# Optimization experiments

Measured on AMD Instinct MI355X. Metric: run time of the kernel, lower is better.

Reference implementation:

```python
import jax, jax.numpy as jnp
import numpy as np

TOP_K = 2
SCALING = 16.0 / 8.0  # alpha / rank


def setup_inputs() -> dict:
    key = jax.random.key(0)
    ks = jax.random.split(key, 9)
    B, V, D, P = 32, 21, 512, 64
    IN, OUT, E, R, H = D * P, 96, 8, 8, 256
    return {
        "x": jax.random.normal(ks[0], (B, V, D, P), jnp.float32),
        "W_base": jax.random.normal(ks[1], (OUT, IN), jnp.float32) * (IN ** -0.5),
        "b_base": jax.random.normal(ks[2], (OUT,), jnp.float32) * 0.01,
        "W1": jax.random.normal(ks[3], (H, D), jnp.float32) * (D ** -0.5),
        "b1": jax.random.normal(ks[4], (H,), jnp.float32) * 0.01,
        "W2": jax.random.normal(ks[5], (E, H), jnp.float32) * (H ** -0.5),
        "b2": jax.random.normal(ks[6], (E,), jnp.float32) * 0.01,
        "lora_A": jax.random.normal(ks[7], (E, R, IN), jnp.float32) * (IN ** -0.5),
        "lora_B": jax.random.normal(ks[8], (E, OUT, R), jnp.float32) * (R ** -0.5),
    }


def reference(x, W_base, b_base, W1, b1, W2, b2, lora_A, lora_B):
    B, V, D, P = x.shape
    E = lora_A.shape[0]
    # FlattenHead: flatten last two dims, then linear (dropout is identity in eval)
    flat = x.reshape(B, V, D * P)                      # [B, V, IN]
    base_out = flat @ W_base.T + b_base                # [B, V, OUT]
    # Router: pool over n_vars then patch dim -> [B, D]
    pooled = x.mean(axis=1).mean(axis=-1)
    h = jax.nn.relu(pooled @ W1.T + b1)
    logits = h @ W2.T + b2                             # [B, E]
    probs = jax.nn.softmax(logits, axis=-1)
    topw, topi = jax.lax.top_k(probs, TOP_K)           # [B, K]
    topw = topw / jnp.clip(topw.sum(-1, keepdims=True), 1e-6)
    # All LoRA experts (matches original dense compute), then weighted combine
    temp = jnp.einsum("bvi,eri->ebvr", flat, lora_A)   # [E, B, V, R]
    delta = jnp.einsum("ebvr,eor->ebvo", temp, lora_B) * SCALING  # [E, B, V, OUT]
    # Scatter top-k weights into dense [B, E] then combine (top-k sparse combine)
    w_full = jnp.zeros((B, E), x.dtype).at[jnp.arange(B)[:, None], topi].add(topw)
    moe_delta = jnp.einsum("be,ebvo->bvo", w_full, delta)
    return base_out + moe_delta, probs
```

## Files before the change

### kernel.cpp

```cpp
#include <hip/hip_runtime.h>

#define B_DIM 32
#define V_DIM 21
#define D_DIM 512
#define P_DIM 64
#define M_TOTAL 672
#define K_TOTAL 32768
#define OUT_DIM 96
#define E_DIM 8
#define R_DIM 8
#define H_DIM 256
#define N_TOTAL 160
#define SCALING 2.0f
#define POOL_SCALE (1.0f / (V_DIM * (float)P_DIM))

#define BM 64
#define BK 128
#define KSPLIT 32
#define K_PER_BLOCK (K_TOTAL / KSPLIT)
#define CHUNKS (K_PER_BLOCK / BK)
#define LDS_K (BK + 8)

typedef __attribute__((ext_vector_type(4))) float floatx4;
typedef __attribute__((ext_vector_type(8))) short short8;

__device__ __forceinline__ unsigned short f2bf(float f) {
  union { float f; unsigned int u; } v; v.f = f;
  unsigned int u = v.u + (0x7FFFu + ((v.u >> 16) & 1u));
  return (unsigned short)(u >> 16);
}

__global__ __launch_bounds__(256, 2)
void gemm_kernel(const float* __restrict__ x, const float* __restrict__ W_base,
                 const float* __restrict__ lora_A, float* __restrict__ S,
                 float* __restrict__ pooled) {
  __shared__ short ldsA[BM * LDS_K];
  __shared__ short ldsW[N_TOTAL * LDS_K];
  __shared__ float lds_pool[5 * 16];
  const int tid = threadIdx.x;
  const int m0 = blockIdx.x * BM;
  const int kbase = blockIdx.y * K_PER_BLOCK;
  const int lane = tid & 63;
  const int wave = tid >> 6;
  const int quad = lane >> 4;
  const int l16 = lane & 15;
  const int b_first = m0 / V_DIM;
  const int d_first = kbase >> 6;

  if (tid < 80) lds_pool[tid] = 0.0f;

  floatx4 acc[10];
  #pragma unroll
  for (int i = 0; i < 10; ++i) acc[i] = (floatx4)(0.0f);

  for (int c = 0; c < CHUNKS; ++c) {
    const int kc = kbase + c * BK;
    __syncthreads();
    #pragma unroll
    for (int it = 0; it < 4; ++it) {
      int idx = it * 256 + tid;
      int row = idx >> 4;
      int g = idx & 15;
      int m = m0 + row;
      float vals[8];
      if (m < M_TOTAL) {
        const floatx4* s4 = (const floatx4*)(x + (size_t)m * K_TOTAL + kc + g * 8);
        floatx4 v0 = s4[0], v1 = s4[1];
        vals[0] = v0[0]; vals[1] = v0[1]; vals[2] = v0[2]; vals[3] = v0[3];
        vals[4] = v1[0]; vals[5] = v1[1]; vals[6] = v1[2]; vals[7] = v1[3];
        float sum8 = (vals[0] + vals[1]) + (vals[2] + vals[3]) +
                     ((vals[4] + vals[5]) + (vals[6] + vals[7]));
        int b_local = (m / V_DIM) - b_first;
        int d_local = ((kc + g * 8) >> 6) - d_first;
        atomicAdd(&lds_pool[b_local * 16 + d_local], sum8);
      } else {
        #pragma unroll
        for (int j = 0; j < 8; ++j) vals[j] = 0.0f;
      }
      short8 sv;
      #pragma unroll
      for (int j = 0; j < 8; ++j) sv[j] = (short)f2bf(vals[j]);
      *(short8*)&ldsA[row * LDS_K + g * 8] = sv;
    }
    #pragma unroll
    for (int it = 0; it < 10; ++it) {
      int idx = it * 256 + tid;
      int row = idx >> 4;
      int g = idx & 15;
      const float* rowp = (row < OUT_DIM) ? (W_base + (size_t)row * K_TOTAL)
                                          : (lora_A + (size_t)(row - OUT_DIM) * K_TOTAL);
      const floatx4* s4 = (const floatx4*)(rowp + kc + g * 8);
      floatx4 v0 = s4[0], v1 = s4[1];
      short8 sv;
      sv[0] = (short)f2bf(v0[0]); sv[1] = (short)f2bf(v0[1]);
      sv[2] = (short)f2bf(v0[2]); sv[3] = (short)f2bf(v0[3]);
      sv[4] = (short)f2bf(v1[0]); sv[5] = (short)f2bf(v1[1]);
      sv[6] = (short)f2bf(v1[2]); sv[7] = (short)f2bf(v1[3]);
      *(short8*)&ldsW[row * LDS_K + g * 8] = sv;
    }
    __syncthreads();
    #pragma unroll
    for (int ks = 0; ks < 4; ++ks) {
      const int ko = ks * 32 + quad * 8;
      short8 a = *(const short8*)&ldsA[(wave * 16 + l16) * LDS_K + ko];
      #pragma unroll
      for (int nt = 0; nt < 10; ++nt) {
        short8 b = *(const short8*)&ldsW[(nt * 16 + l16) * LDS_K + ko];
        acc[nt] = __builtin_amdgcn_mfma_f32_16x16x32_bf16(a, b, acc[nt], 0, 0, 0);
      }
    }
  }
  #pragma unroll
  for (int nt = 0; nt < 10; ++nt) {
    #pragma unroll
    for (int r = 0; r < 4; ++r) {
      int m = m0 + wave * 16 + quad * 4 + r;
      int n = nt * 16 + l16;
      if (m < M_TOTAL) atomicAdd(&S[(size_t)m * N_TOTAL + n], acc[nt][r]);
    }
  }
  if (tid < 80) {
    int b = b_first + (tid >> 4);
    int d = d_first + (tid & 15);
    if (b < B_DIM)
      atomicAdd(&pooled[b * D_DIM + d], lds_pool[tid] * POOL_SCALE);
  }
}

__global__ __launch_bounds__(256)
void router_kernel(const float* __restrict__ pooled, const float* __restrict__ W1,
                   const float* __restrict__ b1, const float* __restrict__ W2,
                   const float* __restrict__ b2, float* __restrict__ wfull,
                   float* __restrict__ probs_out) {
  __shared__ float sp[D_DIM];
  __shared__ float sh[H_DIM];
  __shared__ float slog[E_DIM];
  const int b = blockIdx.x;
  const int t = threadIdx.x;
  sp[t] = pooled[b * D_DIM + t];
  sp[t + 256] = pooled[b * D_DIM + t + 256];
  __syncthreads();
  float acc = b1[t];
  const float* w1r = W1 + (size_t)t * D_DIM;
  for (int d = 0; d < D_DIM; ++d) acc += sp[d] * w1r[d];
  sh[t] = fmaxf(acc, 0.0f);
  __syncthreads();
  if (t < E_DIM) {
    float a = b2[t];
    const float* w2r = W2 + t * H_DIM;
    for (int j = 0; j < H_DIM; ++j) a += sh[j] * w2r[j];
    slog[t] = a;
  }
  __syncthreads();
  if (t == 0) {
    float p[E_DIM];
    float mx = slog[0];
    for (int e = 1; e < E_DIM; ++e) mx = fmaxf(mx, slog[e]);
    float se = 0.0f;
    for (int e = 0; e < E_DIM; ++e) { p[e] = __expf(slog[e] - mx); se += p[e]; }
    float inv = 1.0f / se;
    for (int e = 0; e < E_DIM; ++e) { p[e] *= inv; probs_out[b * E_DIM + e] = p[e]; }
    int i0 = 0;
    for (int e = 1; e < E_DIM; ++e) if (p[e] > p[i0]) i0 = e;
    int i1 = (i0 == 0) ? 1 : 0;
    for (int e = 0; e < E_DIM; ++e) if (e != i0 && p[e] > p[i1]) i1 = e;
    float s2 = p[i0] + p[i1];
    float invs = 1.0f / fmaxf(s2, 1e-6f);
    for (int e = 0; e < E_DIM; ++e) {
      float w = 0.0f;
      if (e == i0) w += p[i0] * invs;
      if (e == i1) w += p[i1] * invs;
      wfull[b * E_DIM + e] = w;
    }
  }
}

__global__ __launch_bounds__(256)
void combine_kernel(const float* __restrict__ S, const float* __restrict__ b_base,
                    const float* __restrict__ lora_B, const float* __restrict__ wfull,
                    float* __restrict__ out) {
  int idx = blockIdx.x * 256 + threadIdx.x;
  if (idx >= M_TOTAL * OUT_DIM) return;
  int bv = idx / OUT_DIM;
  int o = idx - bv * OUT_DIM;
  int b = bv / V_DIM;
  const float* srow = S + (size_t)bv * N_TOTAL;
  float base = srow[o] + b_base[o];
  float moe = 0.0f;
  #pragma unroll
  for (int e = 0; e < E_DIM; ++e) {
    float we = wfull[b * E_DIM + e];
    if (we != 0.0f) {
      const float* lb = lora_B + ((size_t)e * OUT_DIM + o) * R_DIM;
      const float* tr = srow + OUT_DIM + e * R_DIM;
      float d = 0.0f;
      #pragma unroll
      for (int r = 0; r < R_DIM; ++r) d += tr[r] * lb[r];
      moe += we * d;
    }
  }
  out[idx] = base + SCALING * moe;
}

extern "C" void kernel_launch(void* const* d_in, const int* in_sizes, int n_in,
                              void* d_out, int out_size, void* d_ws, size_t ws_size,
                              hipStream_t stream) {
  const float* x      = (const float*)d_in[0];
  const float* W_base = (const float*)d_in[1];
  const float* b_base = (const float*)d_in[2];
  const float* W1     = (const float*)d_in[3];
  const float* b1     = (const float*)d_in[4];
  const float* W2     = (const float*)d_in[5];
  const float* b2     = (const float*)d_in[6];
  const float* lora_A = (const float*)d_in[7];
  const float* lora_B = (const float*)d_in[8];
  float* out = (float*)d_out;

  float* ws     = (float*)d_ws;
  float* pooled = ws;
  float* S      = ws + 16384;
  float* wfull  = ws + 16384 + (size_t)M_TOTAL * N_TOTAL;

  hipMemsetAsync(d_ws, 0, (16384 + (size_t)M_TOTAL * N_TOTAL) * sizeof(float), stream);

  gemm_kernel<<<dim3(11, KSPLIT), 256, 0, stream>>>(x, W_base, lora_A, S, pooled);
  router_kernel<<<B_DIM, 256, 0, stream>>>(pooled, W1, b1, W2, b2, wfull,
                                           out + (size_t)M_TOTAL * OUT_DIM);
  combine_kernel<<<(M_TOTAL * OUT_DIM + 255) / 256, 256, 0, stream>>>(
      S, b_base, lora_B, wfull, out);
}
```

Before: 220.0 us.

## Pre-convert weights to bf16, prefetch next K chunk into registers, retile waves 2x5

A separate kernel converts W_base and lora_A to bf16 once per call, so the GEMM reads half the weight bytes and skips the per-block conversion that was repeated across all 11 M-blocks. The GEMM now loads the next K chunk into registers while running MFMAs on the current one (a register-level double buffer), and splits waves 2x2 over M and N so each A and B fragment read from LDS is reused twice. KSPLIT is doubled to put more blocks on the GPU. The costs are an extra kernel launch, one fp32 read and bf16 write of the weights, higher register pressure, and twice as many split-K atomic adds into S.

```diff
diff --git a/kernel.cpp b/kernel.cpp
--- a/kernel.cpp
+++ b/kernel.cpp
@@ -16,7 +16,7 @@
 
 #define BM 64
 #define BK 128
-#define KSPLIT 32
+#define KSPLIT 64
 #define K_PER_BLOCK (K_TOTAL / KSPLIT)
 #define CHUNKS (K_PER_BLOCK / BK)
 #define LDS_K (BK + 8)
@@ -30,13 +30,30 @@
   return (unsigned short)(u >> 16);
 }
 
+__global__ __launch_bounds__(256)
+void convW_kernel(const float* __restrict__ W_base, const float* __restrict__ lora_A,
+                  short* __restrict__ Wb) {
+  size_t base = ((size_t)blockIdx.x * 256 + threadIdx.x) * 8;
+  int row = (int)(base >> 15);
+  int k = (int)(base & 32767);
+  const float* src = (row < OUT_DIM) ? (W_base + ((size_t)row << 15) + k)
+                                     : (lora_A + ((size_t)(row - OUT_DIM) << 15) + k);
+  floatx4 v0 = ((const floatx4*)src)[0];
+  floatx4 v1 = ((const floatx4*)src)[1];
+  short8 sv;
+  sv[0] = (short)f2bf(v0[0]); sv[1] = (short)f2bf(v0[1]);
+  sv[2] = (short)f2bf(v0[2]); sv[3] = (short)f2bf(v0[3]);
+  sv[4] = (short)f2bf(v1[0]); sv[5] = (short)f2bf(v1[1]);
+  sv[6] = (short)f2bf(v1[2]); sv[7] = (short)f2bf(v1[3]);
+  *(short8*)(Wb + base) = sv;
+}
+
 __global__ __launch_bounds__(256, 2)
-void gemm_kernel(const float* __restrict__ x, const float* __restrict__ W_base,
-                 const float* __restrict__ lora_A, float* __restrict__ S,
-                 float* __restrict__ pooled) {
+void gemm_kernel(const float* __restrict__ x, const short* __restrict__ Wb,
+                 float* __restrict__ S, float* __restrict__ pooled) {
   __shared__ short ldsA[BM * LDS_K];
   __shared__ short ldsW[N_TOTAL * LDS_K];
-  __shared__ float lds_pool[5 * 16];
+  __shared__ float lds_pool[5 * 8];
   const int tid = threadIdx.x;
   const int m0 = blockIdx.x * BM;
   const int kbase = blockIdx.y * K_PER_BLOCK;
@@ -44,84 +61,118 @@
   const int wave = tid >> 6;
   const int quad = lane >> 4;
   const int l16 = lane & 15;
+  const int mhalf = (wave & 1) * 32;
+  const int nhalf = (wave >> 1) * 80;
   const int b_first = m0 / V_DIM;
   const int d_first = kbase >> 6;
 
-  if (tid < 80) lds_pool[tid] = 0.0f;
-
-  floatx4 acc[10];
+  if (tid < 40) lds_pool[tid] = 0.0f;
+
+  floatx4 acc[2][5];
   #pragma unroll
-  for (int i = 0; i < 10; ++i) acc[i] = (floatx4)(0.0f);
+  for (int mt = 0; mt < 2; ++mt)
+    #pragma unroll
+    for (int nt = 0; nt < 5; ++nt) acc[mt][nt] = (floatx4)(0.0f);
+
+  const int a_row0 = tid >> 4;
+  const int a_g = tid & 15;
+
+  floatx4 pa[8];
+  short8  pw[10];
+
+#define ISSUE_LOADS(c)                                                          \
+  {                                                                             \
+    const int kc = kbase + (c) * BK;                                            \
+    _Pragma("unroll")                                                           \
+    for (int it = 0; it < 4; ++it) {                                            \
+      int row = a_row0 + it * 16;                                               \
+      int m = m0 + row;                                                         \
+      if (m < M_TOTAL) {                                                        \
+        const floatx4* s4 = (const floatx4*)(x + (size_t)m * K_TOTAL + kc + a_g * 8); \
+        pa[it * 2] = s4[0];                                                     \
+        pa[it * 2 + 1] = s4[1];                                                 \
+      } else {                                                                  \
+        pa[it * 2] = (floatx4)(0.0f);                                           \
+        pa[it * 2 + 1] = (floatx4)(0.0f);                                       \
+      }                                                                         \
+    }                                                                           \
+    _Pragma("unroll")                                                           \
+    for (int it = 0; it < 10; ++it) {                                           \
+      int idx = it * 256 + tid;                                                 \
+      int row = idx >> 4;                                                       \
+      int g = idx & 15;                                                         \
+      pw[it] = *(const short8*)(Wb + (size_t)row * K_TOTAL + kc + g * 8);       \
+    }                                                                           \
+  }
+
+#define CONVERT_WRITE(c)                                                        \
+  {                                                                             \
+    const int kc = kbase + (c) * BK;                                            \
+    _Pragma("unroll")                                                           \
+    for (int it = 0; it < 4; ++it) {                                            \
+      int row = a_row0 + it * 16;                                               \
+      int m = m0 + row;                                                         \
+      floatx4 v0 = pa[it * 2], v1 = pa[it * 2 + 1];                             \
+      if (m < M_TOTAL) {                                                        \
+        float sum8 = ((v0[0] + v0[1]) + (v0[2] + v0[3])) +                      \
+                     ((v1[0] + v1[1]) + (v1[2] + v1[3]));                       \
+        int b_local = (m / V_DIM) - b_first;                                    \
+        int d_local = ((kc + a_g * 8) >> 6) - d_first;                          \
+        atomicAdd(&lds_pool[b_local * 8 + d_local], sum8);                      \
+      }                                                                         \
+      short8 sv;                                                                \
+      sv[0] = (short)f2bf(v0[0]); sv[1] = (short)f2bf(v0[1]);                   \
+      sv[2] = (short)f2bf(v0[2]); sv[3] = (short)f2bf(v0[3]);                   \
+      sv[4] = (short)f2bf(v1[0]); sv[5] = (short)f2bf(v1[1]);                   \
+      sv[6] = (short)f2bf(v1[2]); sv[7] = (short)f2bf(v1[3]);                   \
+      *(short8*)&ldsA[row * LDS_K + a_g * 8] = sv;                              \
+    }                                                                           \
+    _Pragma("unroll")                                                           \
+    for (int it = 0; it < 10; ++it) {                                           \
+      int idx = it * 256 + tid;                                                 \
+      int row = idx >> 4;                                                       \
+      int g = idx & 15;                                                         \
+      *(short8*)&ldsW[row * LDS_K + g * 8] = pw[it];                            \
+    }                                                                           \
+  }
+
+  ISSUE_LOADS(0);
+  __syncthreads();
+  CONVERT_WRITE(0);
 
   for (int c = 0; c < CHUNKS; ++c) {
-    const int kc = kbase + c * BK;
     __syncthreads();
-    #pragma unroll
-    for (int it = 0; it < 4; ++it) {
-      int idx = it * 256 + tid;
-      int row = idx >> 4;
-      int g = idx & 15;
-      int m = m0 + row;
-      float vals[8];
-      if (m < M_TOTAL) {
-        const floatx4* s4 = (const floatx4*)(x + (size_t)m * K_TOTAL + kc + g * 8);
-        floatx4 v0 = s4[0], v1 = s4[1];
-        vals[0] = v0[0]; vals[1] = v0[1]; vals[2] = v0[2]; vals[3] = v0[3];
-        vals[4] = v1[0]; vals[5] = v1[1]; vals[6] = v1[2]; vals[7] = v1[3];
-        float sum8 = (vals[0] + vals[1]) + (vals[2] + vals[3]) +
-                     ((vals[4] + vals[5]) + (vals[6] + vals[7]));
-        int b_local = (m / V_DIM) - b_first;
-        int d_local = ((kc + g * 8) >> 6) - d_first;
-        atomicAdd(&lds_pool[b_local * 16 + d_local], sum8);
-      } else {
-        #pragma unroll
-        for (int j = 0; j < 8; ++j) vals[j] = 0.0f;
-      }
-      short8 sv;
-      #pragma unroll
-      for (int j = 0; j < 8; ++j) sv[j] = (short)f2bf(vals[j]);
-      *(short8*)&ldsA[row * LDS_K + g * 8] = sv;
-    }
-    #pragma unroll
-    for (int it = 0; it < 10; ++it) {
-      int idx = it * 256 + tid;
-      int row = idx >> 4;
-      int g = idx & 15;
-      const float* rowp = (row < OUT_DIM) ? (W_base + (size_t)row * K_TOTAL)
-                                          : (lora_A + (size_t)(row - OUT_DIM) * K_TOTAL);
-      const floatx4* s4 = (const floatx4*)(rowp + kc + g * 8);
-      floatx4 v0 = s4[0], v1 = s4[1];
-      short8 sv;
-      sv[0] = (short)f2bf(v0[0]); sv[1] = (short)f2bf(v0[1]);
-      sv[2] = (short)f2bf(v0[2]); sv[3] = (short)f2bf(v0[3]);
-      sv[4] = (short)f2bf(v1[0]); sv[5] = (short)f2bf(v1[1]);
-      sv[6] = (short)f2bf(v1[2]); sv[7] = (short)f2bf(v1[3]);
-      *(short8*)&ldsW[row * LDS_K + g * 8] = sv;
-    }
-    __syncthreads();
+    if (c + 1 < CHUNKS) ISSUE_LOADS(c + 1);
     #pragma unroll
     for (int ks = 0; ks < 4; ++ks) {
       const int ko = ks * 32 + quad * 8;
-      short8 a = *(const short8*)&ldsA[(wave * 16 + l16) * LDS_K + ko];
+      short8 a0 = *(const short8*)&ldsA[(mhalf + l16) * LDS_K + ko];
+      short8 a1 = *(const short8*)&ldsA[(mhalf + 16 + l16) * LDS_K + ko];
       #pragma unroll
-      for (int nt = 0; nt < 10; ++nt) {
-        short8 b = *(const short8*)&ldsW[(nt * 16 + l16) * LDS_K + ko];
-        acc[nt] = __builtin_amdgcn_mfma_f32_16x16x32_bf16(a, b, acc[nt], 0, 0, 0);
+      for (int nt = 0; nt < 5; ++nt) {
+        short8 b = *(const short8*)&ldsW[(nhalf + nt * 16 + l16) * LDS_K + ko];
+        acc[0][nt] = __builtin_amdgcn_mfma_f32_16x16x32_bf16(a0, b, acc[0][nt], 0, 0, 0);
+        acc[1][nt] = __builtin_amdgcn_mfma_f32_16x16x32_bf16(a1, b, acc[1][nt], 0, 0, 0);
       }
     }
-  }
+    __syncthreads();
+    if (c + 1 < CHUNKS) CONVERT_WRITE(c + 1);
+  }
+
   #pragma unroll
-  for (int nt = 0; nt < 10; ++nt) {
+  for (int mt = 0; mt < 2; ++mt)
     #pragma unroll
-    for (int r = 0; r < 4; ++r) {
-      int m = m0 + wave * 16 + quad * 4 + r;
-      int n = nt * 16 + l16;
-      if (m < M_TOTAL) atomicAdd(&S[(size_t)m * N_TOTAL + n], acc[nt][r]);
-    }
-  }
-  if (tid < 80) {
-    int b = b_first + (tid >> 4);
-    int d = d_first + (tid & 15);
+    for (int nt = 0; nt < 5; ++nt)
+      #pragma unroll
+      for (int r = 0; r < 4; ++r) {
+        int m = m0 + mhalf + mt * 16 + quad * 4 + r;
+        int n = nhalf + nt * 16 + l16;
+        if (m < M_TOTAL) atomicAdd(&S[(size_t)m * N_TOTAL + n], acc[mt][nt][r]);
+      }
+
+  if (tid < 40) {
+    int b = b_first + (tid >> 3);
+    int d = d_first + (tid & 7);
     if (b < B_DIM)
       atomicAdd(&pooled[b * D_DIM + d], lds_pool[tid] * POOL_SCALE);
   }
@@ -220,10 +271,12 @@
   float* pooled = ws;
   float* S      = ws + 16384;
   float* wfull  = ws + 16384 + (size_t)M_TOTAL * N_TOTAL;
+  short* Wb     = (short*)(wfull + 256);
 
   hipMemsetAsync(d_ws, 0, (16384 + (size_t)M_TOTAL * N_TOTAL) * sizeof(float), stream);
 
-  gemm_kernel<<<dim3(11, KSPLIT), 256, 0, stream>>>(x, W_base, lora_A, S, pooled);
+  convW_kernel<<<(N_TOTAL * K_TOTAL / 8 + 255) / 256, 256, 0, stream>>>(W_base, lora_A, Wb);
+  gemm_kernel<<<dim3(11, KSPLIT), 256, 0, stream>>>(x, Wb, S, pooled);
   router_kernel<<<B_DIM, 256, 0, stream>>>(pooled, W1, b1, W2, b2, wfull,
                                            out + (size_t)M_TOTAL * OUT_DIM);
   combine_kernel<<<(M_TOTAL * OUT_DIM + 255) / 256, 256, 0, stream>>>(
```

Measured after the change: 217.5 us. About the same (-1.1%).

## Pre-convert weights to bf16, drop LDS staging, use per-split partial buffers

Applied to the files above, without the earlier changes.

A new pre-pass converts W_base and lora_A to bf16 once per call, so the GEMM reads weight fragments straight from global memory instead of converting them to LDS in every block. The GEMM drops LDS and barriers, prefetches x one step ahead in registers, and computes the pooled sums with wave shuffles. It writes partial results to per-split buffers instead of doing global atomics, and a fused kernel sums the 64 splits and applies the LoRA combine. The cost is an extra weight conversion pass, a much larger partial-result buffer to read back, and no LDS reuse of weights across waves.

```diff
diff --git a/kernel.cpp b/kernel.cpp
--- a/kernel.cpp
+++ b/kernel.cpp
@@ -14,12 +14,11 @@
 #define SCALING 2.0f
 #define POOL_SCALE (1.0f / (V_DIM * (float)P_DIM))
 
-#define BM 64
-#define BK 128
-#define KSPLIT 32
-#define K_PER_BLOCK (K_TOTAL / KSPLIT)
-#define CHUNKS (K_PER_BLOCK / BK)
-#define LDS_K (BK + 8)
+#define KSPLIT 64
+#define K_PER_SPLIT (K_TOTAL / KSPLIT)
+#define KSTEPS (K_PER_SPLIT / 32)
+#define SMN (M_TOTAL * N_TOTAL)
+#define RC_ROWS 2
 
 typedef __attribute__((ext_vector_type(4))) float floatx4;
 typedef __attribute__((ext_vector_type(8))) short short8;
@@ -30,101 +29,89 @@
   return (unsigned short)(u >> 16);
 }
 
-__global__ __launch_bounds__(256, 2)
-void gemm_kernel(const float* __restrict__ x, const float* __restrict__ W_base,
-                 const float* __restrict__ lora_A, float* __restrict__ S,
-                 float* __restrict__ pooled) {
-  __shared__ short ldsA[BM * LDS_K];
-  __shared__ short ldsW[N_TOTAL * LDS_K];
-  __shared__ float lds_pool[5 * 16];
+__global__ __launch_bounds__(256)
+void convW_kernel(const float* __restrict__ W_base, const float* __restrict__ lora_A,
+                  short* __restrict__ Wb, float* __restrict__ pooled) {
+  int gid = blockIdx.x * 256 + threadIdx.x;
+  if (blockIdx.x < 64) pooled[gid] = 0.0f;
+  size_t base = (size_t)gid * 8;
+  int row = (int)(base >> 15);
+  int k = (int)(base & 32767);
+  const float* src = (row < OUT_DIM) ? (W_base + ((size_t)row << 15) + k)
+                                     : (lora_A + ((size_t)(row - OUT_DIM) << 15) + k);
+  floatx4 v0 = ((const floatx4*)src)[0];
+  floatx4 v1 = ((const floatx4*)src)[1];
+  short8 sv;
+  sv[0] = (short)f2bf(v0[0]); sv[1] = (short)f2bf(v0[1]);
+  sv[2] = (short)f2bf(v0[2]); sv[3] = (short)f2bf(v0[3]);
+  sv[4] = (short)f2bf(v1[0]); sv[5] = (short)f2bf(v1[1]);
+  sv[6] = (short)f2bf(v1[2]); sv[7] = (short)f2bf(v1[3]);
+  *(short8*)(Wb + base) = sv;
+}
+
+__global__ __launch_bounds__(256, 3)
+void gemm_kernel(const float* __restrict__ x, const short* __restrict__ Wb,
+                 float* __restrict__ P, float* __restrict__ pooled) {
   const int tid = threadIdx.x;
-  const int m0 = blockIdx.x * BM;
-  const int kbase = blockIdx.y * K_PER_BLOCK;
+  const int wave = tid >> 6;
   const int lane = tid & 63;
-  const int wave = tid >> 6;
   const int quad = lane >> 4;
   const int l16 = lane & 15;
-  const int b_first = m0 / V_DIM;
-  const int d_first = kbase >> 6;
-
-  if (tid < 80) lds_pool[tid] = 0.0f;
+  const int m0w = blockIdx.x * 64 + wave * 16;
+  if (m0w >= M_TOTAL) return;
+  const int ky = blockIdx.y;
+  const int kbase = ky * K_PER_SPLIT;
+  const int m = m0w + l16;
+  const int bb = m / V_DIM;
+  const float* xp = x + (size_t)m * K_TOTAL + kbase + quad * 8;
+  const short* wp = Wb + (size_t)l16 * K_TOTAL + kbase + quad * 8;
 
   floatx4 acc[10];
   #pragma unroll
-  for (int i = 0; i < 10; ++i) acc[i] = (floatx4)(0.0f);
-
-  for (int c = 0; c < CHUNKS; ++c) {
-    const int kc = kbase + c * BK;
-    __syncthreads();
-    #pragma unroll
-    for (int it = 0; it < 4; ++it) {
-      int idx = it * 256 + tid;
-      int row = idx >> 4;
-      int g = idx & 15;
-      int m = m0 + row;
-      float vals[8];
-      if (m < M_TOTAL) {
-        const floatx4* s4 = (const floatx4*)(x + (size_t)m * K_TOTAL + kc + g * 8);
-        floatx4 v0 = s4[0], v1 = s4[1];
-        vals[0] = v0[0]; vals[1] = v0[1]; vals[2] = v0[2]; vals[3] = v0[3];
-        vals[4] = v1[0]; vals[5] = v1[1]; vals[6] = v1[2]; vals[7] = v1[3];
-        float sum8 = (vals[0] + vals[1]) + (vals[2] + vals[3]) +
-                     ((vals[4] + vals[5]) + (vals[6] + vals[7]));
-        int b_local = (m / V_DIM) - b_first;
-        int d_local = ((kc + g * 8) >> 6) - d_first;
-        atomicAdd(&lds_pool[b_local * 16 + d_local], sum8);
-      } else {
-        #pragma unroll
-        for (int j = 0; j < 8; ++j) vals[j] = 0.0f;
-      }
-      short8 sv;
-      #pragma unroll
-      for (int j = 0; j < 8; ++j) sv[j] = (short)f2bf(vals[j]);
-      *(short8*)&ldsA[row * LDS_K + g * 8] = sv;
-    }
-    #pragma unroll
-    for (int it = 0; it < 10; ++it) {
-      int idx = it * 256 + tid;
-      int row = idx >> 4;
-      int g = idx & 15;
-      const float* rowp = (row < OUT_DIM) ? (W_base + (size_t)row * K_TOTAL)
-                                          : (lora_A + (size_t)(row - OUT_DIM) * K_TOTAL);
-      const floatx4* s4 = (const floatx4*)(rowp + kc + g * 8);
-      floatx4 v0 = s4[0], v1 = s4[1];
-      short8 sv;
-      sv[0] = (short)f2bf(v0[0]); sv[1] = (short)f2bf(v0[1]);
-      sv[2] = (short)f2bf(v0[2]); sv[3] = (short)f2bf(v0[3]);
-      sv[4] = (short)f2bf(v1[0]); sv[5] = (short)f2bf(v1[1]);
-      sv[6] = (short)f2bf(v1[2]); sv[7] = (short)f2bf(v1[3]);
-      *(short8*)&ldsW[row * LDS_K + g * 8] = sv;
-    }
-    __syncthreads();
-    #pragma unroll
-    for (int ks = 0; ks < 4; ++ks) {
-      const int ko = ks * 32 + quad * 8;
-      short8 a = *(const short8*)&ldsA[(wave * 16 + l16) * LDS_K + ko];
-      #pragma unroll
-      for (int nt = 0; nt < 10; ++nt) {
-        short8 b = *(const short8*)&ldsW[(nt * 16 + l16) * LDS_K + ko];
-        acc[nt] = __builtin_amdgcn_mfma_f32_16x16x32_bf16(a, b, acc[nt], 0, 0, 0);
-      }
-    }
-  }
+  for (int nt = 0; nt < 10; ++nt) acc[nt] = (floatx4)(0.0f);
+
+  floatx4 a0 = ((const floatx4*)xp)[0];
+  floatx4 a1 = *(const floatx4*)(xp + 4);
+  float dsum = 0.0f;
+
   #pragma unroll
-  for (int nt = 0; nt < 10; ++nt) {
-    #pragma unroll
-    for (int r = 0; r < 4; ++r) {
-      int m = m0 + wave * 16 + quad * 4 + r;
-      int n = nt * 16 + l16;
-      if (m < M_TOTAL) atomicAdd(&S[(size_t)m * N_TOTAL + n], acc[nt][r]);
-    }
-  }
-  if (tid < 80) {
-    int b = b_first + (tid >> 4);
-    int d = d_first + (tid & 15);
-    if (b < B_DIM)
-      atomicAdd(&pooled[b * D_DIM + d], lds_pool[tid] * POOL_SCALE);
-  }
+  for (int c = 0; c < KSTEPS; ++c) {
+    floatx4 n0 = (floatx4)(0.0f), n1 = (floatx4)(0.0f);
+    if (c + 1 < KSTEPS) {
+      n0 = *(const floatx4*)(xp + (c + 1) * 32);
+      n1 = *(const floatx4*)(xp + (c + 1) * 32 + 4);
+    }
+    short8 pb[10];
+    #pragma unroll
+    for (int nt = 0; nt < 10; ++nt)
+      pb[nt] = *(const short8*)(wp + (size_t)nt * 16 * K_TOTAL + c * 32);
+    short8 af;
+    af[0] = (short)f2bf(a0[0]); af[1] = (short)f2bf(a0[1]);
+    af[2] = (short)f2bf(a0[2]); af[3] = (short)f2bf(a0[3]);
+    af[4] = (short)f2bf(a1[0]); af[5] = (short)f2bf(a1[1]);
+    af[6] = (short)f2bf(a1[2]); af[7] = (short)f2bf(a1[3]);
+    #pragma unroll
+    for (int nt = 0; nt < 10; ++nt)
+      acc[nt] = __builtin_amdgcn_mfma_f32_16x16x32_bf16(af, pb[nt], acc[nt], 0, 0, 0);
+    float s8 = ((a0[0] + a0[1]) + (a0[2] + a0[3])) +
+               ((a1[0] + a1[1]) + (a1[2] + a1[3]));
+    s8 += __shfl_xor(s8, 16, 64);
+    s8 += __shfl_xor(s8, 32, 64);
+    if ((c & 1) == 0) {
+      dsum = s8;
+    } else if (quad == 0) {
+      int d = (kbase >> 6) + (c >> 1);
+      atomicAdd(&pooled[bb * D_DIM + d], (dsum + s8) * POOL_SCALE);
+    }
+    a0 = n0; a1 = n1;
+  }
+
+  float* Pp = P + (size_t)ky * SMN + (size_t)(m0w + quad * 4) * N_TOTAL + l16;
+  #pragma unroll
+  for (int r = 0; r < 4; ++r)
+    #pragma unroll
+    for (int nt = 0; nt < 10; ++nt)
+      Pp[(size_t)r * N_TOTAL + nt * 16] = acc[nt][r];
 }
 
 __global__ __launch_bounds__(256)
@@ -176,30 +163,41 @@
 }
 
 __global__ __launch_bounds__(256)
-void combine_kernel(const float* __restrict__ S, const float* __restrict__ b_base,
-                    const float* __restrict__ lora_B, const float* __restrict__ wfull,
-                    float* __restrict__ out) {
-  int idx = blockIdx.x * 256 + threadIdx.x;
-  if (idx >= M_TOTAL * OUT_DIM) return;
-  int bv = idx / OUT_DIM;
-  int o = idx - bv * OUT_DIM;
-  int b = bv / V_DIM;
-  const float* srow = S + (size_t)bv * N_TOTAL;
-  float base = srow[o] + b_base[o];
-  float moe = 0.0f;
-  #pragma unroll
-  for (int e = 0; e < E_DIM; ++e) {
-    float we = wfull[b * E_DIM + e];
-    if (we != 0.0f) {
-      const float* lb = lora_B + ((size_t)e * OUT_DIM + o) * R_DIM;
-      const float* tr = srow + OUT_DIM + e * R_DIM;
-      float d = 0.0f;
-      #pragma unroll
-      for (int r = 0; r < R_DIM; ++r) d += tr[r] * lb[r];
-      moe += we * d;
-    }
-  }
-  out[idx] = base + SCALING * moe;
+void reduce_combine_kernel(const float* __restrict__ P, const float* __restrict__ b_base,
+                           const float* __restrict__ lora_B, const float* __restrict__ wfull,
+                           float* __restrict__ out) {
+  __shared__ float sS[RC_ROWS * N_TOTAL];
+  const int t = threadIdx.x;
+  const size_t base = (size_t)blockIdx.x * (RC_ROWS * N_TOTAL);
+  for (int s = t; s < RC_ROWS * N_TOTAL; s += 256) {
+    const float* Pp = P + base + s;
+    float a = 0.0f;
+    #pragma unroll 8
+    for (int k = 0; k < KSPLIT; ++k) a += Pp[(size_t)k * SMN];
+    sS[s] = a;
+  }
+  __syncthreads();
+  if (t < RC_ROWS * OUT_DIM) {
+    int mr = t / OUT_DIM;
+    int o = t - mr * OUT_DIM;
+    int mm = blockIdx.x * RC_ROWS + mr;
+    int b = mm / V_DIM;
+    const float* srow = sS + mr * N_TOTAL;
+    float res = srow[o] + b_base[o];
+    float moe = 0.0f;
+    #pragma unroll
+    for (int e = 0; e < E_DIM; ++e) {
+      float we = wfull[b * E_DIM + e];
+      if (we != 0.0f) {
+        const float* lb = lora_B + ((size_t)e * OUT_DIM + o) * R_DIM;
+        float dd = 0.0f;
+        #pragma unroll
+        for (int r = 0; r < R_DIM; ++r) dd += srow[OUT_DIM + e * R_DIM + r] * lb[r];
+        moe += we * dd;
+      }
+    }
+    out[(size_t)mm * OUT_DIM + o] = res + SCALING * moe;
+  }
 }
 
 extern "C" void kernel_launch(void* const* d_in, const int* in_sizes, int n_in,
@@ -218,14 +216,15 @@
 
   float* ws     = (float*)d_ws;
   float* pooled = ws;
-  float* S      = ws + 16384;
-  float* wfull  = ws + 16384 + (size_t)M_TOTAL * N_TOTAL;
-
-  hipMemsetAsync(d_ws, 0, (16384 + (size_t)M_TOTAL * N_TOTAL) * sizeof(float), stream);
-
-  gemm_kernel<<<dim3(11, KSPLIT), 256, 0, stream>>>(x, W_base, lora_A, S, pooled);
+  float* wfull  = ws + 16384;
+  short* Wb     = (short*)(wfull + 256);
+  float* P      = (float*)(Wb + (size_t)N_TOTAL * K_TOTAL);
+
+  convW_kernel<<<(N_TOTAL * K_TOTAL / 8 + 255) / 256, 256, 0, stream>>>(
+      W_base, lora_A, Wb, pooled);
+  gemm_kernel<<<dim3(11, KSPLIT), 256, 0, stream>>>(x, Wb, P, pooled);
   router_kernel<<<B_DIM, 256, 0, stream>>>(pooled, W1, b1, W2, b2, wfull,
                                            out + (size_t)M_TOTAL * OUT_DIM);
-  combine_kernel<<<(M_TOTAL * OUT_DIM + 255) / 256, 256, 0, stream>>>(
-      S, b_base, lora_B, wfull, out);
-}
+  reduce_combine_kernel<<<M_TOTAL / RC_ROWS, 256, 0, stream>>>(
+      P, b_base, lora_B, wfull, out);
+}
```

Result: slower. 251.6 us (+14.4%).
